# Kernel tuning notes

Measured on AMD Instinct MI355X. Metric: run time of the kernel, lower is better.

The kernel has to match this reference:

```python
import jax, jax.numpy as jnp
import numpy as np

N = 1048576   # nodes (1024x1024 fluid grid)
E = 8388608   # edges (avg degree 8)
IDX_NODE_X, IDX_NODE_Y = 0, 1
IDX_EDGE_X, IDX_EDGE_Y = 0, 1


def setup_inputs() -> dict:
    key = jax.random.key(0)
    ks = jax.random.split(key, 9)
    v_x = jax.random.normal(ks[0], (N, 2), jnp.float32)
    v_prev_x = jax.random.normal(ks[1], (N, 2), jnp.float32)
    p_x = jax.random.normal(ks[2], (N, 1), jnp.float32)
    p_prev_x = jax.random.normal(ks[3], (N, 1), jnp.float32)
    rho_x = jax.random.normal(ks[4], (N, 1), jnp.float32)
    rho_prev_x = jax.random.normal(ks[5], (N, 1), jnp.float32)
    edge_attr = jax.random.normal(ks[6], (E, 2), jnp.float32)
    # mimic grid finite-difference sparsity: ~half the entries of each
    # direction column are exactly zero, exercising the != 0 edge masking
    keep = jax.random.bernoulli(ks[7], 0.5, (E, 2))
    edge_attr = jnp.where(keep, edge_attr, 0.0)
    edge_index = jax.random.randint(ks[8], (2, E), 0, N, dtype=jnp.int64)
    return dict(
        v_x=v_x, v_prev_x=v_prev_x, p_x=p_x, p_prev_x=p_prev_x,
        rho_x=rho_x, rho_prev_x=rho_prev_x,
        M=jnp.float32(1.0), eta=jnp.float32(1.0), zeta=jnp.float32(1.0),
        dt=jnp.float32(0.01), edge_attr=edge_attr, edge_index=edge_index,
    )


def _spatial_derivative(x, src, dst, edge_attr, mask, idx_node, idx_edge, n):
    """Gather-compute-scatter finite difference: scatter-mean of
    (x[dst, idx_node] - x[src, idx_node]) / edge_attr[:, idx_edge]
    over the masked edge subset, aggregated at the source node."""
    diff = x[dst, idx_node] - x[src, idx_node]                  # [E]
    denom = jnp.where(mask, edge_attr[:, idx_edge], 1.0)        # avoid /0 on masked-out edges
    contrib = jnp.where(mask, diff / denom, 0.0)                # [E]
    sums = jax.ops.segment_sum(contrib, src, num_segments=n)    # [N]
    cnt = jax.ops.segment_sum(mask.astype(x.dtype), src, num_segments=n)
    return sums / jnp.maximum(cnt, 1.0)                         # [N]


def reference(v_x, v_prev_x, p_x, p_prev_x, rho_x, rho_prev_x, M, eta, zeta, dt, edge_attr, edge_index):
    n = v_x.shape[0]
    src, dst = edge_index[0], edge_index[1]
    vp = v_x * p_x                                  # [N,2] * [N,1] -> [N,2]
    mask_x = edge_attr[:, IDX_NODE_X] != 0          # edges with x-offset
    mask_y = edge_attr[:, IDX_NODE_Y] != 0          # edges with y-offset
    d_x = _spatial_derivative(vp, src, dst, edge_attr, mask_x, IDX_NODE_X, IDX_EDGE_X, n)
    d_y = _spatial_derivative(vp, src, dst, edge_attr, mask_y, IDX_NODE_Y, IDX_EDGE_Y, n)
    loss_continuity = (d_x + d_y)[:, None] + (p_x - p_prev_x) / dt   # [N,1]
    return loss_continuity
```

## Files before the change

### kernel.cpp

```cpp
#include <hip/hip_runtime.h>
#include <hip/hip_fp16.h>


#define NPB      2048
#define NPB_LOG  11
#define NBUCK_MAX 512
#define CE       4096
#define CB       1024
#define EPT      4
#define CCAP     3456
#define MAXCHUNK 2048
#define NHINT    4096
#define SPILLCAP (1 << 18)
#define K_OFF    1073741824.0

typedef unsigned long long ull;

struct __align__(4) Rec12 { unsigned m; float ax, ay; };


__global__ void node_pre_fast(const float2* __restrict__ v,
                              const float* __restrict__ p,
                              __half2* __restrict__ vph,
                              int* __restrict__ spill_cnt, int N) {
    int i = blockIdx.x * blockDim.x + threadIdx.x;
    int stride = gridDim.x * blockDim.x;
    for (; i < N; i += stride) {
        float2 vi = v[i];
        float pi = p[i];
        vph[i] = __float22half2_rn(make_float2(vi.x * pi, vi.y * pi));
    }
    if (blockIdx.x == 0 && threadIdx.x == 0) *spill_cnt = 0;
}

__global__ __launch_bounds__(CB) void chunk_sort(
        const float2* __restrict__ ea,
        const int* __restrict__ src_idx,
        const int* __restrict__ dst_idx,
        Rec12* __restrict__ recs,
        unsigned short* __restrict__ off_mat,
        unsigned short* __restrict__ cnt_mat,
        uint4* __restrict__ spill,
        int* __restrict__ spill_cnt,
        int nbuck, int E) {
    __shared__ Rec12 stage[CCAP];
    __shared__ int hist[NBUCK_MAX];
    __shared__ int tl[NBUCK_MAX];
    __shared__ int cur[NBUCK_MAX];
    int c = blockIdx.x, t = threadIdx.x;
    int e0 = c * CE;

    unsigned M[EPT];
    float AX[EPT], AY[EPT];
    int K[EPT], NR[EPT];
#pragma unroll
    for (int i = 0; i < EPT; ++i) {
        int e = e0 + i * CB + t;
        NR[i] = 0; K[i] = 0;
        if (e < E) {
            float2 a = ea[e];
            if (a.x != 0.f || a.y != 0.f) {
                int s = src_idx[e];
                int d = dst_idx[e];
                K[i] = s >> NPB_LOG;
                M[i] = (unsigned)(s & (NPB - 1)) | ((unsigned)d << NPB_LOG);
                AX[i] = a.x;
                AY[i] = a.y;
                NR[i] = 1;
            }
        }
    }
    if (t < nbuck) hist[t] = 0;
    __syncthreads();
#pragma unroll
    for (int i = 0; i < EPT; ++i)
        if (NR[i]) atomicAdd(&hist[K[i]], 1);
    __syncthreads();
    if (t < nbuck) tl[t] = hist[t];
    __syncthreads();
    for (int off = 1; off < NBUCK_MAX; off <<= 1) {
        int x = 0;
        if (t < nbuck && t >= off) x = tl[t - off];
        __syncthreads();
        if (t < nbuck) tl[t] += x;
        __syncthreads();
    }
    int total = tl[nbuck - 1];
    if (t < nbuck) {
        int excl = tl[t] - hist[t];
        cur[t] = excl;
        off_mat[(size_t)c * nbuck + t] = (unsigned short)excl;
        cnt_mat[(size_t)c * nbuck + t] = (unsigned short)hist[t];
    }
    __syncthreads();
    size_t rb = (size_t)c * CCAP;
    if (total <= CCAP) {
#pragma unroll
        for (int i = 0; i < EPT; ++i)
            if (NR[i]) {
                int slot = atomicAdd(&cur[K[i]], 1);
                stage[slot].m = M[i];
                stage[slot].ax = AX[i];
                stage[slot].ay = AY[i];
            }
        __syncthreads();
        for (int j = t; j < total; j += CB) recs[rb + j] = stage[j];
    } else {
#pragma unroll
        for (int i = 0; i < EPT; ++i)
            if (NR[i]) {
                int slot = atomicAdd(&cur[K[i]], 1);
                if (slot < CCAP) {
                    recs[rb + slot].m = M[i];
                    recs[rb + slot].ax = AX[i];
                    recs[rb + slot].ay = AY[i];
                } else {
                    int sp = atomicAdd(spill_cnt, 1);
                    if (sp < SPILLCAP)
                        spill[sp] = make_uint4(M[i], __float_as_uint(AX[i]),
                                               __float_as_uint(AY[i]), (unsigned)K[i]);
                }
            }
    }
}

__global__ __launch_bounds__(1024) void bucket_reduce(
        const Rec12* __restrict__ recs,
        const unsigned short* __restrict__ off_mat,
        const unsigned short* __restrict__ cnt_mat,
        const float2* __restrict__ v,
        const float* __restrict__ p,
        const __half2* __restrict__ vph,
        const uint4* __restrict__ spill,
        const int* __restrict__ spill_cnt,
        const float* __restrict__ p_prev,
        const float* __restrict__ dt_ptr,
        float* __restrict__ out,
        int nchunk, int nbuck, int N) {
    __shared__ float2 vps[NPB];
    __shared__ double2 acc[NPB];
    __shared__ int glen[MAXCHUNK];
    __shared__ int goff[MAXCHUNK];
    __shared__ unsigned short hint[NHINT];
    __shared__ int s_sp;
    int k = blockIdx.x, t = threadIdx.x;
    int g0 = k * NPB;
    for (int i = t; i < NPB; i += 1024) {
        int g = g0 + i;
        float2 vi = (g < N) ? v[g] : make_float2(0.f, 0.f);
        float pi = (g < N) ? p[g] : 0.f;
        vps[i] = make_float2(vi.x * pi, vi.y * pi);
        acc[i] = make_double2(0.0, 0.0);
    }
    if (t == 0) s_sp = *spill_cnt;
    for (int c = t; c < MAXCHUNK; c += 1024) {
        int len = 0, off = 0;
        if (c < nchunk) {
            off = off_mat[(size_t)c * nbuck + k];
            int cnt = cnt_mat[(size_t)c * nbuck + k];
            len = min(cnt, max(0, CCAP - off));
        }
        goff[c] = off;
        glen[c] = len;
    }
    __syncthreads();
    for (int off = 1; off < MAXCHUNK; off <<= 1) {
        int i0 = t, i1 = t + 1024;
        int x0 = (i0 >= off) ? glen[i0 - off] : 0;
        int x1 = glen[i1 - off];
        __syncthreads();
        glen[i0] += x0;
        glen[i1] += x1;
        __syncthreads();
    }
    int total = glen[MAXCHUNK - 1];
    int nh = min((total + 7) >> 3, NHINT);
    for (int j = t; j < nh; j += 1024) {
        int target = j << 3;
        int lo = 0, hi = nchunk - 1;
        while (lo < hi) {
            int mid = (lo + hi) >> 1;
            if (glen[mid] > target) hi = mid; else lo = mid + 1;
        }
        hint[j] = (unsigned short)lo;
    }
    __syncthreads();
    for (int idx = t; idx < total; idx += 1024) {
        int cur = hint[idx >> 3];
        while (glen[cur] <= idx) ++cur;
        int pre = cur ? glen[cur - 1] : 0;
        Rec12 r = recs[(size_t)cur * CCAP + goff[cur] + (idx - pre)];
        int sl = (int)(r.m & (NPB - 1u));
        int d = (int)(r.m >> NPB_LOG);
        float2 vpd = __half22float2(vph[d]);
        float2 vs = vps[sl];
        if (r.ax != 0.f)
            unsafeAtomicAdd(&acc[sl].x, (double)((vpd.x - vs.x) / r.ax) + K_OFF);
        if (r.ay != 0.f)
            unsafeAtomicAdd(&acc[sl].y, (double)((vpd.y - vs.y) / r.ay) + K_OFF);
    }
    __syncthreads();
    int nsp = min(s_sp, SPILLCAP);
    for (int i = t; i < nsp; i += 1024) {
        uint4 r = spill[i];
        if ((int)r.w != k) continue;
        int sl = (int)(r.x & (NPB - 1u));
        int d = (int)(r.x >> NPB_LOG);
        float ax = __uint_as_float(r.y);
        float ay = __uint_as_float(r.z);
        float2 vpd = __half22float2(vph[d]);
        float2 vs = vps[sl];
        if (ax != 0.f)
            unsafeAtomicAdd(&acc[sl].x, (double)((vpd.x - vs.x) / ax) + K_OFF);
        if (ay != 0.f)
            unsafeAtomicAdd(&acc[sl].y, (double)((vpd.y - vs.y) / ay) + K_OFF);
    }
    if (nsp) __syncthreads();
    float inv_dt = 1.0f / dt_ptr[0];
    for (int i = t; i < NPB; i += 1024) {
        int g = g0 + i;
        if (g < N) {
            double2 A = acc[i];
            double cx = rint(A.x * (1.0 / K_OFF));
            double sx = A.x - cx * K_OFF;
            double cy = rint(A.y * (1.0 / K_OFF));
            double sy = A.y - cy * K_OFF;
            out[g] = (float)(sx / fmax(cx, 1.0)) + (float)(sy / fmax(cy, 1.0))
                   + (p[g] - p_prev[g]) * inv_dt;
        }
    }
}


__global__ void fb_node_pre(const float2* __restrict__ v,
                            const float* __restrict__ p,
                            float2* __restrict__ vp,
                            double2* __restrict__ acc, int N) {
    int i = blockIdx.x * blockDim.x + threadIdx.x;
    int stride = gridDim.x * blockDim.x;
    for (; i < N; i += stride) {
        float2 vi = v[i];
        float pi = p[i];
        vp[i] = make_float2(vi.x * pi, vi.y * pi);
        acc[i] = make_double2(0.0, 0.0);
    }
}

__global__ void fb_edge_scatter(const float2* __restrict__ vp,
                                const float2* __restrict__ ea,
                                const int* __restrict__ src_idx,
                                const int* __restrict__ dst_idx,
                                double2* __restrict__ acc, int E) {
    int e = blockIdx.x * blockDim.x + threadIdx.x;
    if (e >= E) return;
    float2 a = ea[e];
    bool mx = (a.x != 0.f);
    bool my = (a.y != 0.f);
    if (!mx && !my) return;
    int s = src_idx[e];
    int d = dst_idx[e];
    float2 vs = vp[s];
    float2 vd = vp[d];
    double* basep = (double*)&acc[s];
    if (mx) unsafeAtomicAdd(basep + 0, (double)((vd.x - vs.x) / a.x) + K_OFF);
    if (my) unsafeAtomicAdd(basep + 1, (double)((vd.y - vs.y) / a.y) + K_OFF);
}

__global__ void fb_node_final(const double2* __restrict__ acc,
                              const float* __restrict__ p,
                              const float* __restrict__ p_prev,
                              const float* __restrict__ dt_ptr,
                              float* __restrict__ out, int N) {
    int i = blockIdx.x * blockDim.x + threadIdx.x;
    int stride = gridDim.x * blockDim.x;
    float inv_dt = 1.0f / dt_ptr[0];
    for (; i < N; i += stride) {
        double2 A = acc[i];
        double cx = rint(A.x * (1.0 / K_OFF));
        double sx = A.x - cx * K_OFF;
        double cy = rint(A.y * (1.0 / K_OFF));
        double sy = A.y - cy * K_OFF;
        out[i] = (float)(sx / fmax(cx, 1.0)) + (float)(sy / fmax(cy, 1.0))
               + (p[i] - p_prev[i]) * inv_dt;
    }
}


extern "C" void kernel_launch(void* const* d_in, const int* in_sizes, int n_in,
                              void* d_out, int out_size, void* d_ws, size_t ws_size,
                              hipStream_t stream) {
    const float2* v_x    = (const float2*)d_in[0];
    const float*  p_x    = (const float*)d_in[2];
    const float*  p_prev = (const float*)d_in[3];
    const float*  dt     = (const float*)d_in[9];
    const float2* ea     = (const float2*)d_in[10];
    const int*    eidx   = (const int*)d_in[11];

    const int N = in_sizes[2];
    const int E = in_sizes[10] / 2;
    const int* src_idx = eidx;
    const int* dst_idx = eidx + E;

    const int nbuck  = (N + NPB - 1) >> NPB_LOG;
    const int nchunk = (E + CE - 1) / CE;

    char* w = (char*)d_ws;
    __half2* vph      = (__half2*)w;  w += (size_t)N * sizeof(__half2);
    int*     spill_cnt= (int*)w;      w += 16;
    unsigned short* off_mat = (unsigned short*)w;  w += (size_t)nchunk * nbuck * sizeof(unsigned short);
    unsigned short* cnt_mat = (unsigned short*)w;  w += (size_t)nchunk * nbuck * sizeof(unsigned short);
    w = (char*)(((uintptr_t)w + 15) & ~(uintptr_t)15);
    uint4*   spill    = (uint4*)w;    w += (size_t)SPILLCAP * sizeof(uint4);
    Rec12*   recs     = (Rec12*)w;    w += (size_t)nchunk * CCAP * sizeof(Rec12);
    size_t need_fast = (size_t)(w - (char*)d_ws);

    if (nbuck <= NBUCK_MAX && nchunk <= MAXCHUNK && N <= (1 << 20)
        && ws_size >= need_fast) {
        node_pre_fast<<<2048, 256, 0, stream>>>(v_x, p_x, vph, spill_cnt, N);
        chunk_sort<<<nchunk, CB, 0, stream>>>(ea, src_idx, dst_idx,
                                              recs, off_mat, cnt_mat,
                                              spill, spill_cnt, nbuck, E);
        bucket_reduce<<<nbuck, 1024, 0, stream>>>(recs, off_mat, cnt_mat,
                                                  v_x, p_x, vph,
                                                  spill, spill_cnt,
                                                  p_prev, dt,
                                                  (float*)d_out, nchunk, nbuck, N);
    } else {
        float2*  fvp  = (float2*)d_ws;
        double2* facc = (double2*)((char*)d_ws + (size_t)N * sizeof(float2));
        fb_node_pre<<<2048, 256, 0, stream>>>(v_x, p_x, fvp, facc, N);
        fb_edge_scatter<<<(E + 255) / 256, 256, 0, stream>>>(
            fvp, ea, src_idx, dst_idx, facc, E);
        fb_node_final<<<2048, 256, 0, stream>>>(
            facc, p_x, p_prev, dt, (float*)d_out, N);
    }
}
```

Before: 131.1 us.

## Split edge records into SoA arrays and vectorize node premultiply

Replaces the 12-byte array-of-structs edge record with separate arrays for the packed index word and the float2 edge attributes, both in shared staging and in global memory. The record load in the bucket reduce and the stores in the chunk sort become naturally aligned 4- and 8-byte accesses instead of unaligned 12-byte ones. The node premultiply kernel now handles two nodes per thread with float4/float2 loads and 8-byte stores, and the fast path requires an even N. The split adds a second store loop and a second read stream per record.

```diff
diff --git a/kernel.cpp b/kernel.cpp
--- a/kernel.cpp
+++ b/kernel.cpp
@@ -16,19 +16,19 @@
 
 typedef unsigned long long ull;
 
-struct __align__(4) Rec12 { unsigned m; float ax, ay; };
-
-
-__global__ void node_pre_fast(const float2* __restrict__ v,
-                              const float* __restrict__ p,
-                              __half2* __restrict__ vph,
-                              int* __restrict__ spill_cnt, int N) {
+
+__global__ void node_pre_fast(const float4* __restrict__ v2,
+                              const float2* __restrict__ p2,
+                              uint2* __restrict__ vph2,
+                              int* __restrict__ spill_cnt, int N2) {
     int i = blockIdx.x * blockDim.x + threadIdx.x;
     int stride = gridDim.x * blockDim.x;
-    for (; i < N; i += stride) {
-        float2 vi = v[i];
-        float pi = p[i];
-        vph[i] = __float22half2_rn(make_float2(vi.x * pi, vi.y * pi));
+    for (; i < N2; i += stride) {
+        float4 vv = v2[i];
+        float2 pp = p2[i];
+        __half2 h0 = __float22half2_rn(make_float2(vv.x * pp.x, vv.y * pp.x));
+        __half2 h1 = __float22half2_rn(make_float2(vv.z * pp.y, vv.w * pp.y));
+        vph2[i] = make_uint2(*(unsigned*)&h0, *(unsigned*)&h1);
     }
     if (blockIdx.x == 0 && threadIdx.x == 0) *spill_cnt = 0;
 }
@@ -37,13 +37,15 @@
         const float2* __restrict__ ea,
         const int* __restrict__ src_idx,
         const int* __restrict__ dst_idx,
-        Rec12* __restrict__ recs,
+        unsigned* __restrict__ recs_m,
+        float2* __restrict__ recs_a,
         unsigned short* __restrict__ off_mat,
         unsigned short* __restrict__ cnt_mat,
         uint4* __restrict__ spill,
         int* __restrict__ spill_cnt,
         int nbuck, int E) {
-    __shared__ Rec12 stage[CCAP];
+    __shared__ unsigned stage_m[CCAP];
+    __shared__ float2 stage_a[CCAP];
     __shared__ int hist[NBUCK_MAX];
     __shared__ int tl[NBUCK_MAX];
     __shared__ int cur[NBUCK_MAX];
@@ -99,21 +101,20 @@
         for (int i = 0; i < EPT; ++i)
             if (NR[i]) {
                 int slot = atomicAdd(&cur[K[i]], 1);
-                stage[slot].m = M[i];
-                stage[slot].ax = AX[i];
-                stage[slot].ay = AY[i];
+                stage_m[slot] = M[i];
+                stage_a[slot] = make_float2(AX[i], AY[i]);
             }
         __syncthreads();
-        for (int j = t; j < total; j += CB) recs[rb + j] = stage[j];
+        for (int j = t; j < total; j += CB) recs_m[rb + j] = stage_m[j];
+        for (int j = t; j < total; j += CB) recs_a[rb + j] = stage_a[j];
     } else {
 #pragma unroll
         for (int i = 0; i < EPT; ++i)
             if (NR[i]) {
                 int slot = atomicAdd(&cur[K[i]], 1);
                 if (slot < CCAP) {
-                    recs[rb + slot].m = M[i];
-                    recs[rb + slot].ax = AX[i];
-                    recs[rb + slot].ay = AY[i];
+                    recs_m[rb + slot] = M[i];
+                    recs_a[rb + slot] = make_float2(AX[i], AY[i]);
                 } else {
                     int sp = atomicAdd(spill_cnt, 1);
                     if (sp < SPILLCAP)
@@ -125,7 +126,8 @@
 }
 
 __global__ __launch_bounds__(1024) void bucket_reduce(
-        const Rec12* __restrict__ recs,
+        const unsigned* __restrict__ recs_m,
+        const float2* __restrict__ recs_a,
         const unsigned short* __restrict__ off_mat,
         const unsigned short* __restrict__ cnt_mat,
         const float2* __restrict__ v,
@@ -189,15 +191,17 @@
         int cur = hint[idx >> 3];
         while (glen[cur] <= idx) ++cur;
         int pre = cur ? glen[cur - 1] : 0;
-        Rec12 r = recs[(size_t)cur * CCAP + goff[cur] + (idx - pre)];
-        int sl = (int)(r.m & (NPB - 1u));
-        int d = (int)(r.m >> NPB_LOG);
+        size_t ri = (size_t)cur * CCAP + goff[cur] + (idx - pre);
+        unsigned m = recs_m[ri];
+        float2 a2 = recs_a[ri];
+        int sl = (int)(m & (NPB - 1u));
+        int d = (int)(m >> NPB_LOG);
         float2 vpd = __half22float2(vph[d]);
         float2 vs = vps[sl];
-        if (r.ax != 0.f)
-            unsafeAtomicAdd(&acc[sl].x, (double)((vpd.x - vs.x) / r.ax) + K_OFF);
-        if (r.ay != 0.f)
-            unsafeAtomicAdd(&acc[sl].y, (double)((vpd.y - vs.y) / r.ay) + K_OFF);
+        if (a2.x != 0.f)
+            unsafeAtomicAdd(&acc[sl].x, (double)((vpd.x - vs.x) / a2.x) + K_OFF);
+        if (a2.y != 0.f)
+            unsafeAtomicAdd(&acc[sl].y, (double)((vpd.y - vs.y) / a2.y) + K_OFF);
     }
     __syncthreads();
     int nsp = min(s_sp, SPILLCAP);
@@ -311,16 +315,20 @@
     unsigned short* cnt_mat = (unsigned short*)w;  w += (size_t)nchunk * nbuck * sizeof(unsigned short);
     w = (char*)(((uintptr_t)w + 15) & ~(uintptr_t)15);
     uint4*   spill    = (uint4*)w;    w += (size_t)SPILLCAP * sizeof(uint4);
-    Rec12*   recs     = (Rec12*)w;    w += (size_t)nchunk * CCAP * sizeof(Rec12);
+    unsigned* recs_m  = (unsigned*)w; w += (size_t)nchunk * CCAP * sizeof(unsigned);
+    w = (char*)(((uintptr_t)w + 15) & ~(uintptr_t)15);
+    float2*  recs_a   = (float2*)w;   w += (size_t)nchunk * CCAP * sizeof(float2);
     size_t need_fast = (size_t)(w - (char*)d_ws);
 
     if (nbuck <= NBUCK_MAX && nchunk <= MAXCHUNK && N <= (1 << 20)
-        && ws_size >= need_fast) {
-        node_pre_fast<<<2048, 256, 0, stream>>>(v_x, p_x, vph, spill_cnt, N);
+        && (N % 2) == 0 && ws_size >= need_fast) {
+        node_pre_fast<<<2048, 256, 0, stream>>>((const float4*)v_x,
+                                                (const float2*)p_x,
+                                                (uint2*)vph, spill_cnt, N / 2);
         chunk_sort<<<nchunk, CB, 0, stream>>>(ea, src_idx, dst_idx,
-                                              recs, off_mat, cnt_mat,
+                                              recs_m, recs_a, off_mat, cnt_mat,
                                               spill, spill_cnt, nbuck, E);
-        bucket_reduce<<<nbuck, 1024, 0, stream>>>(recs, off_mat, cnt_mat,
+        bucket_reduce<<<nbuck, 1024, 0, stream>>>(recs_m, recs_a, off_mat, cnt_mat,
                                                   v_x, p_x, vph,
                                                   spill, spill_cnt,
                                                   p_prev, dt,
```

After: 154.7 us. 1.18x slower.
